# Kernel optimization log

Measured on AMD Instinct MI355X. Metric: run time of the kernel, lower is better.

The kernel has to match this reference:

```python
import jax, jax.numpy as jnp
import numpy as np

WS = 8        # window_size
NH = 8        # num_heads
LN_EPS = 1e-5

# static relative-position index table [WS*WS, WS*WS], values in [0, (2*WS-1)**2)
def _rel_index(ws):
    coords = np.arange(ws)
    grid = np.stack(np.meshgrid(coords, coords, indexing='ij')).reshape(2, -1)  # [2, W2]
    rel = grid[:, :, None] - grid[:, None, :]            # [2, W2, W2]
    rel = rel.transpose(1, 2, 0).copy()                   # [W2, W2, 2]
    rel[..., 0] += ws - 1
    rel[..., 1] += ws - 1
    rel[..., 0] *= 2 * ws - 1
    return rel.sum(-1)                                    # [W2, W2]

REL_IDX = jnp.asarray(_rel_index(WS))


def _ln(x):
    # LayerNorm without affine params (elementwise_affine=False)
    mu = jnp.mean(x, axis=-1, keepdims=True)
    var = jnp.var(x, axis=-1, keepdims=True)
    return (x - mu) * jax.lax.rsqrt(var + LN_EPS)


def setup_inputs() -> dict:
    key = jax.random.key(0)
    ks = jax.random.split(key, 16)
    B, Hg, Wg, C = 8, 64, 64, 256
    L = Hg * Wg
    s = 0.02
    inp = {
        'x': jax.random.normal(ks[0], (B, L, C), jnp.float32),
        't_embed': jax.random.normal(ks[1], (B, C), jnp.float32),
        'H': Hg,
        'W': Wg,
        'adaln1_w': s * jax.random.normal(ks[2], (C, 2 * C), jnp.float32),
        'adaln1_b': jnp.zeros((2 * C,), jnp.float32),
        'adaln2_w': s * jax.random.normal(ks[3], (C, 2 * C), jnp.float32),
        'adaln2_b': jnp.zeros((2 * C,), jnp.float32),
        'bias_table': s * jax.random.normal(ks[4], ((2 * WS - 1) ** 2, NH), jnp.float32),
        'q_w': s * jax.random.normal(ks[5], (C, C), jnp.float32),
        'q_b': jnp.zeros((C,), jnp.float32),
        'k_w': s * jax.random.normal(ks[6], (C, C), jnp.float32),
        'k_b': jnp.zeros((C,), jnp.float32),
        'v_w': s * jax.random.normal(ks[7], (C, C), jnp.float32),
        'v_b': jnp.zeros((C,), jnp.float32),
        'o_w': s * jax.random.normal(ks[8], (C, C), jnp.float32),
        'o_b': jnp.zeros((C,), jnp.float32),
        'ffn1_w': s * jax.random.normal(ks[9], (C, 4 * C), jnp.float32),
        'ffn1_b': jnp.zeros((4 * C,), jnp.float32),
        'ffn2_w': s * jax.random.normal(ks[10], (4 * C, C), jnp.float32),
        'ffn2_b': jnp.zeros((C,), jnp.float32),
    }
    return inp


def reference(x, t_embed, H, W, adaln1_w, adaln1_b, adaln2_w, adaln2_b,
              bias_table, q_w, q_b, k_w, k_b, v_w, v_b, o_w, o_b,
              ffn1_w, ffn1_b, ffn2_w, ffn2_b):
    B, L, C = x.shape
    d = C // NH
    W2 = WS * WS
    sh = WS // 2  # cyclic shift (shifted=True)

    # --- AdaLN1 ---
    ss = t_embed @ adaln1_w + adaln1_b              # [B, 2C]
    scale, shift = jnp.split(ss, 2, axis=-1)
    xn = _ln(x) * (1.0 + scale[:, None, :]) + shift[:, None, :]

    # --- shifted window partition ---
    xg = xn.reshape(B, H, W, C)
    xg = jnp.roll(xg, (-sh, -sh), axis=(1, 2))
    xw = xg.reshape(B, H // WS, WS, W // WS, WS, C).transpose(0, 1, 3, 2, 4, 5)
    xw = xw.reshape(-1, W2, C)                       # [nwB, W2, C]
    nwB = xw.shape[0]

    # --- window attention with relative position bias ---
    q = (xw @ q_w + q_b).reshape(nwB, W2, NH, d).transpose(0, 2, 1, 3)
    k = (xw @ k_w + k_b).reshape(nwB, W2, NH, d).transpose(0, 2, 1, 3)
    v = (xw @ v_w + v_b).reshape(nwB, W2, NH, d).transpose(0, 2, 1, 3)
    logits = jnp.einsum('whqd,whkd->whqk', q, k) * (d ** -0.5)
    bias = bias_table[REL_IDX.reshape(-1)].reshape(W2, W2, NH).transpose(2, 0, 1)
    logits = logits + bias[None].astype(logits.dtype)
    attn = jax.nn.softmax(logits, axis=-1)
    out = jnp.einsum('whqk,whkd->whqd', attn, v).transpose(0, 2, 1, 3).reshape(nwB, W2, C)
    out = out @ o_w + o_b

    # --- window reverse + unshift ---
    xm = out.reshape(B, H // WS, W // WS, WS, WS, C).transpose(0, 1, 3, 2, 4, 5)
    xm = xm.reshape(B, H, W, C)
    xm = jnp.roll(xm, (sh, sh), axis=(1, 2))
    x = x + xm.reshape(B, L, C)

    # --- AdaLN2 + FFN (GELU exact, matching torch nn.GELU) ---
    ss2 = t_embed @ adaln2_w + adaln2_b
    sc2, sh2 = jnp.split(ss2, 2, axis=-1)
    xn2 = _ln(x) * (1.0 + sc2[:, None, :]) + sh2[:, None, :]
    h = jax.nn.gelu(xn2 @ ffn1_w + ffn1_b, approximate=False)
    x = x + (h @ ffn2_w + ffn2_b)
    return x
```

## Files before the change

### kernel.cpp

```cpp
#include <hip/hip_runtime.h>
#include <math.h>

#define WS_ 8
#define NH_ 8
#define C_ 256
#define B_ 8
#define M_ 32768
#define SH_ 4
#define LN_EPS 1e-5f
#define SL_ 8388608

typedef __attribute__((ext_vector_type(8))) short bf16x8;
typedef __attribute__((ext_vector_type(4))) float f32x4;

__device__ inline float b2f(unsigned short u) {
    union { unsigned int i; float f; } c; c.i = ((unsigned int)u) << 16; return c.f;
}
__device__ inline unsigned short f2b(float f) {
    union { unsigned int i; float f; } c; c.f = f;
    unsigned int u = c.i;
    return (unsigned short)((u + 0x7FFFu + ((u >> 16) & 1u)) >> 16);
}
__device__ inline float gelu_f(float x) {
    float t = 1.59576912160573f * (x + 0.044715f * x * x * x);
    return x / (1.f + __expf(-t));
}

__global__ void prep_k(const float* __restrict__ qw, const float* __restrict__ kw,
                       const float* __restrict__ vw, const float* __restrict__ ow,
                       const float* __restrict__ f1w, const float* __restrict__ f2w,
                       const float* __restrict__ qb, const float* __restrict__ kb,
                       const float* __restrict__ vb, const float* __restrict__ bt,
                       const float* __restrict__ te,
                       const float* __restrict__ a1w, const float* __restrict__ a1b,
                       const float* __restrict__ a2w, const float* __restrict__ a2b,
                       unsigned short* __restrict__ qkvT, unsigned short* __restrict__ oT,
                       unsigned short* __restrict__ f1T, unsigned short* __restrict__ f2T,
                       float* __restrict__ qkvB, float* __restrict__ bias_full,
                       float* __restrict__ ss1, float* __restrict__ ss2) {
    int t = blockIdx.x * 256 + threadIdx.x;
    if (t < 196608) {
        int n = t >> 8, k = t & 255;
        const float* w = n < 256 ? qw : (n < 512 ? kw : vw);
        qkvT[t] = f2b(w[k * 256 + (n & 255)]);
    } else if (t < 262144) {
        int i = t - 196608; int n = i >> 8, k = i & 255;
        oT[i] = f2b(ow[k * 256 + n]);
    } else if (t < 524288) {
        int i = t - 262144; int n = i >> 8, k = i & 255;
        f1T[i] = f2b(f1w[k * 1024 + n]);
    } else if (t < 786432) {
        int i = t - 524288; int n = i >> 10, k = i & 1023;
        f2T[i] = f2b(f2w[k * 256 + n]);
    } else if (t < 787200) {
        int i = t - 786432;
        qkvB[i] = i < 256 ? qb[i] : (i < 512 ? kb[i - 256] : vb[i - 512]);
    } else if (t < 819968) {
        int i = t - 787200;
        int head = i >> 12, qk = i & 4095;
        int q = qk >> 6, k = qk & 63;
        int qh = q >> 3, qw2 = q & 7, kh = k >> 3, kw2 = k & 7;
        bias_full[i] = bt[((qh - kh + 7) * 15 + (qw2 - kw2 + 7)) * 8 + head];
    } else if (t < 828160) {
        int i = t - 819968;
        int which = i >> 12;
        int rem = i & 4095;
        int b = rem >> 9, col = rem & 511;
        const float* w = which ? a2w : a1w;
        const float* bb = which ? a2b : a1b;
        const float* tr = te + b * C_;
        float acc = bb[col];
        for (int k = 0; k < C_; ++k) acc += tr[k] * w[k * 512 + col];
        (which ? ss2 : ss1)[b * 512 + col] = acc;
    }
}

__global__ __launch_bounds__(256) void ln_win_k(const float* __restrict__ x,
                                                const float* __restrict__ ss,
                                                unsigned short* __restrict__ xw) {
    int t = blockIdx.x * 4 + (threadIdx.x >> 6);
    int lane = threadIdx.x & 63;
    int b = t >> 12, rem = t & 4095;
    int hg = rem >> 6, wg = rem & 63;
    int hs = (hg + SH_) & 63, wsrc = (wg + SH_) & 63;
    size_t src = ((size_t)b << 12) + (hs << 6) + wsrc;
    float4 v = *(const float4*)&x[src * C_ + lane * 4];
    float s = v.x + v.y + v.z + v.w;
    float s2 = v.x * v.x + v.y * v.y + v.z * v.z + v.w * v.w;
#pragma unroll
    for (int m = 1; m < 64; m <<= 1) { s += __shfl_xor(s, m); s2 += __shfl_xor(s2, m); }
    float mu = s * (1.f / 256.f);
    float rstd = rsqrtf(s2 * (1.f / 256.f) - mu * mu + LN_EPS);
    float4 sc = *(const float4*)&ss[b * 512 + lane * 4];
    float4 sh = *(const float4*)&ss[b * 512 + 256 + lane * 4];
    int win = (b << 6) + ((hg >> 3) << 3) + (wg >> 3);
    int pos = ((hg & 7) << 3) + (wg & 7);
    ushort4 pk;
    pk.x = f2b((v.x - mu) * rstd * (1.f + sc.x) + sh.x);
    pk.y = f2b((v.y - mu) * rstd * (1.f + sc.y) + sh.y);
    pk.z = f2b((v.z - mu) * rstd * (1.f + sc.z) + sh.z);
    pk.w = f2b((v.w - mu) * rstd * (1.f + sc.w) + sh.w);
    *(ushort4*)(xw + (size_t)(win * 64 + pos) * C_ + lane * 4) = pk;
}

__global__ __launch_bounds__(256) void ln_k(const float* __restrict__ x,
                                            const float* __restrict__ ss,
                                            unsigned short* __restrict__ y_out) {
    int t = blockIdx.x * 4 + (threadIdx.x >> 6);
    int lane = threadIdx.x & 63;
    int b = t >> 12;
    float4 v = *(const float4*)&x[(size_t)t * C_ + lane * 4];
    float s = v.x + v.y + v.z + v.w;
    float s2 = v.x * v.x + v.y * v.y + v.z * v.z + v.w * v.w;
#pragma unroll
    for (int m = 1; m < 64; m <<= 1) { s += __shfl_xor(s, m); s2 += __shfl_xor(s2, m); }
    float mu = s * (1.f / 256.f);
    float rstd = rsqrtf(s2 * (1.f / 256.f) - mu * mu + LN_EPS);
    float4 sc = *(const float4*)&ss[b * 512 + lane * 4];
    float4 sh = *(const float4*)&ss[b * 512 + 256 + lane * 4];
    ushort4 pk;
    pk.x = f2b((v.x - mu) * rstd * (1.f + sc.x) + sh.x);
    pk.y = f2b((v.y - mu) * rstd * (1.f + sc.y) + sh.y);
    pk.z = f2b((v.z - mu) * rstd * (1.f + sc.z) + sh.z);
    pk.w = f2b((v.w - mu) * rstd * (1.f + sc.w) + sh.w);
    *(ushort4*)(y_out + (size_t)t * C_ + lane * 4) = pk;
}

template <int KDIM, int MODE, int NT, int MINW>
__global__ __launch_bounds__(256, MINW) void gemm_bf16_k(
    const unsigned short* __restrict__ A, const unsigned short* __restrict__ Bt,
    const float* __restrict__ bias, const float* __restrict__ res,
    void* __restrict__ Cout, int Nout) {
    __shared__ __align__(16) unsigned short As[2][2][4096];
    __shared__ __align__(16) unsigned short Bs[2][2][4096];
    const int blk = blockIdx.x;
    const int xcd = blk & 7;
    const int idx = blk >> 3;
    const int mt = xcd + ((idx / NT) << 3);
    const int nt = idx % NT;
    const int bm = mt * 128, bn = nt * 128;
    const int tid = threadIdx.x;
    const int w = tid >> 6, lane = tid & 63;
    const int quad = lane >> 4, l16 = lane & 15;
    const int wm = (w >> 1) * 64, wn = (w & 1) * 64;
    const int srow = lane >> 2;
    const int qlog = ((lane & 3) ^ ((lane >> 3) & 3)) << 3;
    const int rsw = ((l16 >> 1) & 3) << 3;

    f32x4 acc[4][4] = {};

    auto stage = [&](int buf, int k0) {
#pragma unroll
        for (int h = 0; h < 2; ++h) {
#pragma unroll
            for (int j = 0; j < 2; ++j) {
                int r = j * 64 + w * 16 + srow;
                const unsigned short* ga = A + (size_t)(bm + r) * KDIM + k0 + h * 32 + qlog;
                unsigned short* la = &As[buf][h][j * 2048 + w * 512 + lane * 8];
                __builtin_amdgcn_global_load_lds(
                    (const __attribute__((address_space(1))) void*)ga,
                    (__attribute__((address_space(3))) void*)la, 16, 0, 0);
                const unsigned short* gb = Bt + (size_t)(bn + r) * KDIM + k0 + h * 32 + qlog;
                unsigned short* lb = &Bs[buf][h][j * 2048 + w * 512 + lane * 8];
                __builtin_amdgcn_global_load_lds(
                    (const __attribute__((address_space(1))) void*)gb,
                    (__attribute__((address_space(3))) void*)lb, 16, 0, 0);
            }
        }
    };

    constexpr int NK = KDIM / 64;
    stage(0, 0);
    asm volatile("s_waitcnt vmcnt(0)" ::: "memory");
    __builtin_amdgcn_s_barrier();

#pragma unroll
    for (int ks = 0; ks < NK; ++ks) {
        const int cur = ks & 1;
        if (ks + 1 < NK) stage(cur ^ 1, (ks + 1) * 64);
#pragma unroll
        for (int h = 0; h < 2; ++h) {
            bf16x8 af[4], bfr[4];
#pragma unroll
            for (int i = 0; i < 4; ++i)
                af[i] = *(const bf16x8*)&As[cur][h][(wm + i * 16 + l16) * 32 + ((quad << 3) ^ rsw)];
#pragma unroll
            for (int j = 0; j < 4; ++j)
                bfr[j] = *(const bf16x8*)&Bs[cur][h][(wn + j * 16 + l16) * 32 + ((quad << 3) ^ rsw)];
#pragma unroll
            for (int i = 0; i < 4; ++i)
#pragma unroll
                for (int j = 0; j < 4; ++j)
                    acc[i][j] = __builtin_amdgcn_mfma_f32_16x16x32_bf16(
                        bfr[j], af[i], acc[i][j], 0, 0, 0);
        }
        if (ks + 1 < NK) {
            asm volatile("s_waitcnt vmcnt(0)" ::: "memory");
            __builtin_amdgcn_s_barrier();
        }
    }

#pragma unroll
    for (int i = 0; i < 4; ++i) {
        const int row = bm + wm + i * 16 + l16;
        size_t rowbase = 0;
        if (MODE == 0) {
            int win = row >> 6, pos = row & 63;
            rowbase = (size_t)win * 16384 + pos * 32;
        } else if (MODE == 1) {
            int win = row >> 6, pos = row & 63;
            int b = win >> 6, wh = (win >> 3) & 7, ww = win & 7;
            int hg = (wh << 3) + (pos >> 3), wg = (ww << 3) + (pos & 7);
            int hd = (hg + SH_) & 63, wd = (wg + SH_) & 63;
            rowbase = (((size_t)b << 12) + (hd << 6) + wd) * C_;
        } else {
            rowbase = (size_t)row * Nout;
        }
#pragma unroll
        for (int j = 0; j < 4; ++j) {
            const int col = bn + wn + j * 16 + quad * 4;
            float4 bv = *(const float4*)&bias[col];
            float v0 = acc[i][j][0] + bv.x, v1 = acc[i][j][1] + bv.y;
            float v2 = acc[i][j][2] + bv.z, v3 = acc[i][j][3] + bv.w;
            if (MODE == 0) {
                int which = col >> 8, head = (col >> 5) & 7, dc = col & 31;
                ushort4 pk = {f2b(v0), f2b(v1), f2b(v2), f2b(v3)};
                *(ushort4*)((unsigned short*)Cout + (size_t)which * SL_ + rowbase +
                            head * 2048 + dc) = pk;
            } else if (MODE == 1) {
                float4 rv = *(const float4*)&res[rowbase + col];
                float4 ov = {v0 + rv.x, v1 + rv.y, v2 + rv.z, v3 + rv.w};
                *(float4*)&((float*)Cout)[rowbase + col] = ov;
            } else if (MODE == 2) {
                ushort4 pk = {f2b(gelu_f(v0)), f2b(gelu_f(v1)),
                              f2b(gelu_f(v2)), f2b(gelu_f(v3))};
                *(ushort4*)((unsigned short*)Cout + rowbase + col) = pk;
            } else {
                float4 rv = *(const float4*)&res[rowbase + col];
                float4 ov = {v0 + rv.x, v1 + rv.y, v2 + rv.z, v3 + rv.w};
                *(float4*)&((float*)Cout)[rowbase + col] = ov;
            }
        }
    }
}

__global__ __launch_bounds__(256) void attn_mfma_k(
    const unsigned short* __restrict__ qkv, const float* __restrict__ bias_full,
    unsigned short* __restrict__ attn_out) {
    __shared__ __align__(16) unsigned short Pb[4][64 * 66];
    __shared__ __align__(16) unsigned short Vt[4][32 * 66];
    const int w = threadIdx.x >> 6, lane = threadIdx.x & 63;
    const int wh = blockIdx.x * 4 + w;
    const int win = wh >> 3, head = wh & 7;
    const int quad = lane >> 4, l16 = lane & 15;

    const unsigned short* qp = qkv + (size_t)win * 16384 + head * 2048;
    const unsigned short* kp = qp + SL_;
    const unsigned short* vp = qp + 2 * (size_t)SL_;

    {
        const uint4* v4 = (const uint4*)(vp + lane * 32);
        unsigned short* dst = &Vt[w][0];
#pragma unroll
        for (int c = 0; c < 4; ++c) {
            uint4 u = v4[c];
            unsigned int uu[4] = {u.x, u.y, u.z, u.w};
#pragma unroll
            for (int p = 0; p < 4; ++p) {
                int d0 = c * 8 + p * 2;
                dst[d0 * 66 + lane] = (unsigned short)(uu[p] & 0xffff);
                dst[(d0 + 1) * 66 + lane] = (unsigned short)(uu[p] >> 16);
            }
        }
    }

    bf16x8 qf[4], kf[4];
#pragma unroll
    for (int i = 0; i < 4; ++i) {
        qf[i] = *(const bf16x8*)(qp + (i * 16 + l16) * 32 + quad * 8);
        kf[i] = *(const bf16x8*)(kp + (i * 16 + l16) * 32 + quad * 8);
    }

    f32x4 s[4][4] = {};
#pragma unroll
    for (int i = 0; i < 4; ++i)
#pragma unroll
        for (int j = 0; j < 4; ++j)
            s[i][j] = __builtin_amdgcn_mfma_f32_16x16x32_bf16(qf[i], kf[j], s[i][j], 0, 0, 0);

    const float scale = 0.17677669529663687f;
    const float* bf = bias_full + head * 4096;
    float rs[4][4];
#pragma unroll
    for (int i = 0; i < 4; ++i) {
#pragma unroll
        for (int r = 0; r < 4; ++r) {
            int row = i * 16 + quad * 4 + r;
            float acc = 0.f;
#pragma unroll
            for (int j = 0; j < 4; ++j) {
                float e = __expf(s[i][j][r] * scale + bf[row * 64 + j * 16 + l16]);
                s[i][j][r] = e;
                acc += e;
            }
#pragma unroll
            for (int msk = 1; msk < 16; msk <<= 1) acc += __shfl_xor(acc, msk);
            rs[i][r] = 1.f / acc;
        }
    }

#pragma unroll
    for (int i = 0; i < 4; ++i)
#pragma unroll
        for (int j = 0; j < 4; ++j)
#pragma unroll
            for (int r = 0; r < 4; ++r)
                Pb[w][(i * 16 + quad * 4 + r) * 66 + j * 16 + l16] = f2b(s[i][j][r]);

    __syncthreads();

    f32x4 o[4][2] = {};
#pragma unroll
    for (int st = 0; st < 2; ++st) {
        bf16x8 bv[2];
#pragma unroll
        for (int jo = 0; jo < 2; ++jo)
            bv[jo] = *(const bf16x8*)&Vt[w][(jo * 16 + l16) * 66 + st * 32 + quad * 8];
#pragma unroll
        for (int i = 0; i < 4; ++i) {
            bf16x8 af = *(const bf16x8*)&Pb[w][(i * 16 + l16) * 66 + st * 32 + quad * 8];
#pragma unroll
            for (int jo = 0; jo < 2; ++jo)
                o[i][jo] = __builtin_amdgcn_mfma_f32_16x16x32_bf16(af, bv[jo], o[i][jo], 0, 0, 0);
        }
    }

#pragma unroll
    for (int i = 0; i < 4; ++i)
#pragma unroll
        for (int jo = 0; jo < 2; ++jo)
#pragma unroll
            for (int r = 0; r < 4; ++r) {
                int row = i * 16 + quad * 4 + r;
                int d = jo * 16 + l16;
                attn_out[((size_t)(win * 64 + row)) * C_ + head * 32 + d] =
                    f2b(o[i][jo][r] * rs[i][r]);
            }
}

extern "C" void kernel_launch(void* const* d_in, const int* in_sizes, int n_in,
                              void* d_out, int out_size, void* d_ws, size_t ws_size,
                              hipStream_t stream) {
    const float* x        = (const float*)d_in[0];
    const float* t_embed  = (const float*)d_in[1];
    const float* adaln1_w = (const float*)d_in[4];
    const float* adaln1_b = (const float*)d_in[5];
    const float* adaln2_w = (const float*)d_in[6];
    const float* adaln2_b = (const float*)d_in[7];
    const float* bt       = (const float*)d_in[8];
    const float* q_w = (const float*)d_in[9],  *q_b = (const float*)d_in[10];
    const float* k_w = (const float*)d_in[11], *k_b = (const float*)d_in[12];
    const float* v_w = (const float*)d_in[13], *v_b = (const float*)d_in[14];
    const float* o_w = (const float*)d_in[15], *o_b = (const float*)d_in[16];
    const float* f1_w = (const float*)d_in[17], *f1_b = (const float*)d_in[18];
    const float* f2_w = (const float*)d_in[19], *f2_b = (const float*)d_in[20];
    float* out = (float*)d_out;

    char* wsb = (char*)d_ws;
    float* ss1            = (float*)(wsb + 0);
    float* ss2            = (float*)(wsb + 16384);
    float* qkvB           = (float*)(wsb + 32768);
    unsigned short* qkvT  = (unsigned short*)(wsb + 36864);
    unsigned short* oT    = (unsigned short*)(wsb + 430080);
    unsigned short* f1T   = (unsigned short*)(wsb + 561152);
    unsigned short* f2T   = (unsigned short*)(wsb + 1085440);
    float* bias_full      = (float*)(wsb + 1609728);
    unsigned short* xw    = (unsigned short*)(wsb + 2097152);
    unsigned short* qkv   = (unsigned short*)(wsb + 18874368);
    unsigned short* attn  = (unsigned short*)(wsb + 69206016);
    unsigned short* xn2   = xw;
    unsigned short* hbuf  = qkv;
    float* x1             = (float*)(wsb + 85983232);

    prep_k<<<3235, 256, 0, stream>>>(q_w, k_w, v_w, o_w, f1_w, f2_w, q_b, k_b, v_b, bt,
                                     t_embed, adaln1_w, adaln1_b, adaln2_w, adaln2_b,
                                     qkvT, oT, f1T, f2T, qkvB, bias_full, ss1, ss2);
    ln_win_k<<<8192, 256, 0, stream>>>(x, ss1, xw);

    gemm_bf16_k<256, 0, 6, 2><<<1536, 256, 0, stream>>>(xw, qkvT, qkvB, nullptr, qkv, 768);

    attn_mfma_k<<<1024, 256, 0, stream>>>(qkv, bias_full, attn);

    gemm_bf16_k<256, 1, 2, 2><<<512, 256, 0, stream>>>(attn, oT, o_b, x, x1, 256);
    ln_k<<<8192, 256, 0, stream>>>(x1, ss2, xn2);
    gemm_bf16_k<256, 2, 8, 2><<<2048, 256, 0, stream>>>(xn2, f1T, f1_b, nullptr, hbuf, 1024);
    gemm_bf16_k<1024, 3, 2, 2><<<512, 256, 0, stream>>>(hbuf, f2T, f2_b, x1, out, 256);
}
```

Measured before the change: 276.5 us.

## Restructure GEMMs with full-K A tiles in LDS, direct B loads, and fused LN2

Replaces the 128x128 double-buffered GEMM with a 512-thread kernel that computes 128x256 output tiles. Each block stages a full 256-wide K chunk of A into swizzled LDS and reads B fragments straight from global memory. The O-projection GEMM now covers a full row of 256 columns, so it also computes LayerNorm plus AdaLN2 in its epilogue through an LDS reduction, and the separate ln_k kernel is removed. This saves one launch and one full read of x1. The cost is a 64KB+ LDS footprint that limits occupancy, and uncached B reads from global memory may add latency.

Result: slower. 317.4 us (+14.8%).

```diff
diff --git a/kernel.cpp b/kernel.cpp
--- a/kernel.cpp
+++ b/kernel.cpp
@@ -103,122 +103,176 @@
     *(ushort4*)(xw + (size_t)(win * 64 + pos) * C_ + lane * 4) = pk;
 }
 
-__global__ __launch_bounds__(256) void ln_k(const float* __restrict__ x,
-                                            const float* __restrict__ ss,
-                                            unsigned short* __restrict__ y_out) {
-    int t = blockIdx.x * 4 + (threadIdx.x >> 6);
-    int lane = threadIdx.x & 63;
-    int b = t >> 12;
-    float4 v = *(const float4*)&x[(size_t)t * C_ + lane * 4];
-    float s = v.x + v.y + v.z + v.w;
-    float s2 = v.x * v.x + v.y * v.y + v.z * v.z + v.w * v.w;
-#pragma unroll
-    for (int m = 1; m < 64; m <<= 1) { s += __shfl_xor(s, m); s2 += __shfl_xor(s2, m); }
-    float mu = s * (1.f / 256.f);
-    float rstd = rsqrtf(s2 * (1.f / 256.f) - mu * mu + LN_EPS);
-    float4 sc = *(const float4*)&ss[b * 512 + lane * 4];
-    float4 sh = *(const float4*)&ss[b * 512 + 256 + lane * 4];
-    ushort4 pk;
-    pk.x = f2b((v.x - mu) * rstd * (1.f + sc.x) + sh.x);
-    pk.y = f2b((v.y - mu) * rstd * (1.f + sc.y) + sh.y);
-    pk.z = f2b((v.z - mu) * rstd * (1.f + sc.z) + sh.z);
-    pk.w = f2b((v.w - mu) * rstd * (1.f + sc.w) + sh.w);
-    *(ushort4*)(y_out + (size_t)t * C_ + lane * 4) = pk;
-}
-
-template <int KDIM, int MODE, int NT, int MINW>
-__global__ __launch_bounds__(256, MINW) void gemm_bf16_k(
+template <int KDIM, int MODE, int NT>
+__global__ __launch_bounds__(512, 2) void gemmv_k(
     const unsigned short* __restrict__ A, const unsigned short* __restrict__ Bt,
     const float* __restrict__ bias, const float* __restrict__ res,
-    void* __restrict__ Cout, int Nout) {
-    __shared__ __align__(16) unsigned short As[2][2][4096];
-    __shared__ __align__(16) unsigned short Bs[2][2][4096];
+    void* __restrict__ Cout, const float* __restrict__ ss2,
+    unsigned short* __restrict__ xn2out, int Nout) {
+    constexpr int NCH = KDIM / 256;
+    constexpr int NBUF = (NCH > 1) ? 2 : 1;
+    __shared__ __align__(16) unsigned short As[NBUF][128 * 256];
+
     const int blk = blockIdx.x;
     const int xcd = blk & 7;
     const int idx = blk >> 3;
     const int mt = xcd + ((idx / NT) << 3);
     const int nt = idx % NT;
-    const int bm = mt * 128, bn = nt * 128;
+    const int bm = mt * 128, bn = nt * 256;
     const int tid = threadIdx.x;
     const int w = tid >> 6, lane = tid & 63;
     const int quad = lane >> 4, l16 = lane & 15;
-    const int wm = (w >> 1) * 64, wn = (w & 1) * 64;
-    const int srow = lane >> 2;
-    const int qlog = ((lane & 3) ^ ((lane >> 3) & 3)) << 3;
-    const int rsw = ((l16 >> 1) & 3) << 3;
+    const int wrow = (w >> 2) * 64;
+    const int wcol = (w & 3) * 64;
+    const int srow16 = tid >> 5;
+    const int sc = tid & 31;
 
     f32x4 acc[4][4] = {};
 
-    auto stage = [&](int buf, int k0) {
-#pragma unroll
-        for (int h = 0; h < 2; ++h) {
-#pragma unroll
-            for (int j = 0; j < 2; ++j) {
-                int r = j * 64 + w * 16 + srow;
-                const unsigned short* ga = A + (size_t)(bm + r) * KDIM + k0 + h * 32 + qlog;
-                unsigned short* la = &As[buf][h][j * 2048 + w * 512 + lane * 8];
-                __builtin_amdgcn_global_load_lds(
-                    (const __attribute__((address_space(1))) void*)ga,
-                    (__attribute__((address_space(3))) void*)la, 16, 0, 0);
-                const unsigned short* gb = Bt + (size_t)(bn + r) * KDIM + k0 + h * 32 + qlog;
-                unsigned short* lb = &Bs[buf][h][j * 2048 + w * 512 + lane * 8];
-                __builtin_amdgcn_global_load_lds(
-                    (const __attribute__((address_space(1))) void*)gb,
-                    (__attribute__((address_space(3))) void*)lb, 16, 0, 0);
-            }
+    auto stageA = [&](int buf, int kc) {
+#pragma unroll
+        for (int p = 0; p < 8; ++p) {
+            int row = p * 16 + srow16;
+            int g = sc ^ (row & 7);
+            const unsigned short* ga = A + (size_t)(bm + row) * KDIM + kc * 256 + g * 8;
+            unsigned short* la = &As[buf][row * 256 + sc * 8];
+            __builtin_amdgcn_global_load_lds(
+                (const __attribute__((address_space(1))) void*)ga,
+                (__attribute__((address_space(3))) void*)la, 16, 0, 0);
         }
     };
 
-    constexpr int NK = KDIM / 64;
-    stage(0, 0);
-    asm volatile("s_waitcnt vmcnt(0)" ::: "memory");
-    __builtin_amdgcn_s_barrier();
-
-#pragma unroll
-    for (int ks = 0; ks < NK; ++ks) {
-        const int cur = ks & 1;
-        if (ks + 1 < NK) stage(cur ^ 1, (ks + 1) * 64);
-#pragma unroll
-        for (int h = 0; h < 2; ++h) {
-            bf16x8 af[4], bfr[4];
-#pragma unroll
-            for (int i = 0; i < 4; ++i)
-                af[i] = *(const bf16x8*)&As[cur][h][(wm + i * 16 + l16) * 32 + ((quad << 3) ^ rsw)];
+    auto computeC = [&](int buf, int kc) {
+        const unsigned short* bp = Bt + (size_t)(bn + wcol + l16) * KDIM + kc * 256 + quad * 8;
+#pragma unroll
+        for (int k8 = 0; k8 < 8; ++k8) {
+            bf16x8 bfr[4], af[4];
 #pragma unroll
             for (int j = 0; j < 4; ++j)
-                bfr[j] = *(const bf16x8*)&Bs[cur][h][(wn + j * 16 + l16) * 32 + ((quad << 3) ^ rsw)];
+                bfr[j] = *(const bf16x8*)(bp + (size_t)j * 16 * KDIM + k8 * 32);
+#pragma unroll
+            for (int i = 0; i < 4; ++i) {
+                int row = wrow + i * 16 + l16;
+                int cidx = (k8 * 4 + quad) ^ (row & 7);
+                af[i] = *(const bf16x8*)&As[buf][row * 256 + cidx * 8];
+            }
+            __builtin_amdgcn_s_setprio(1);
 #pragma unroll
             for (int i = 0; i < 4; ++i)
 #pragma unroll
                 for (int j = 0; j < 4; ++j)
                     acc[i][j] = __builtin_amdgcn_mfma_f32_16x16x32_bf16(
                         bfr[j], af[i], acc[i][j], 0, 0, 0);
-        }
-        if (ks + 1 < NK) {
-            asm volatile("s_waitcnt vmcnt(0)" ::: "memory");
-            __builtin_amdgcn_s_barrier();
-        }
+            __builtin_amdgcn_s_setprio(0);
+        }
+    };
+
+    stageA(0, 0);
+    asm volatile("s_waitcnt vmcnt(0)" ::: "memory");
+    __builtin_amdgcn_s_barrier();
+    if constexpr (NCH == 1) {
+        computeC(0, 0);
+    } else {
+#pragma unroll
+        for (int c = 0; c < NCH; ++c) {
+            if (c + 1 < NCH) stageA((c + 1) & 1, c + 1);
+            computeC(c & 1, c);
+            if (c + 1 < NCH) {
+                asm volatile("s_waitcnt vmcnt(0)" ::: "memory");
+                __builtin_amdgcn_s_barrier();
+            }
+        }
+    }
+
+    if (MODE == 1) {
+        float ps[4], ps2[4];
+#pragma unroll
+        for (int i = 0; i < 4; ++i) {
+            const int row = bm + wrow + i * 16 + l16;
+            int win = row >> 6, pos = row & 63;
+            int b = win >> 6, wh = (win >> 3) & 7, ww = win & 7;
+            int hg = (wh << 3) + (pos >> 3), wg = (ww << 3) + (pos & 7);
+            int hd = (hg + SH_) & 63, wd = (wg + SH_) & 63;
+            size_t rowbase = (((size_t)b << 12) + (hd << 6) + wd) * C_;
+            float s = 0.f, s2 = 0.f;
+#pragma unroll
+            for (int j = 0; j < 4; ++j) {
+                const int col = bn + wcol + j * 16 + quad * 4;
+                float4 bv = *(const float4*)&bias[col];
+                float4 rv = *(const float4*)&res[rowbase + col];
+                float4 ov = {acc[i][j][0] + bv.x + rv.x, acc[i][j][1] + bv.y + rv.y,
+                             acc[i][j][2] + bv.z + rv.z, acc[i][j][3] + bv.w + rv.w};
+                *(float4*)&((float*)Cout)[rowbase + col] = ov;
+                acc[i][j][0] = ov.x; acc[i][j][1] = ov.y;
+                acc[i][j][2] = ov.z; acc[i][j][3] = ov.w;
+                s += ov.x + ov.y + ov.z + ov.w;
+                s2 += ov.x * ov.x + ov.y * ov.y + ov.z * ov.z + ov.w * ov.w;
+            }
+            ps[i] = s; ps2[i] = s2;
+        }
+#pragma unroll
+        for (int i = 0; i < 4; ++i) {
+            ps[i] += __shfl_xor(ps[i], 16);  ps[i] += __shfl_xor(ps[i], 32);
+            ps2[i] += __shfl_xor(ps2[i], 16); ps2[i] += __shfl_xor(ps2[i], 32);
+        }
+        float* sred = (float*)&As[0][0];
+        asm volatile("s_waitcnt lgkmcnt(0)" ::: "memory");
+        __builtin_amdgcn_s_barrier();
+        if (quad == 0) {
+#pragma unroll
+            for (int i = 0; i < 4; ++i) {
+                int r = i * 16 + l16;
+                sred[(w * 64 + r) * 2 + 0] = ps[i];
+                sred[(w * 64 + r) * 2 + 1] = ps2[i];
+            }
+        }
+        __builtin_amdgcn_s_barrier();
+#pragma unroll
+        for (int i = 0; i < 4; ++i) {
+            int r = i * 16 + l16;
+            float s = 0.f, s2 = 0.f;
+#pragma unroll
+            for (int cw = 0; cw < 4; ++cw) {
+                s  += sred[(((w >> 2) * 4 + cw) * 64 + r) * 2 + 0];
+                s2 += sred[(((w >> 2) * 4 + cw) * 64 + r) * 2 + 1];
+            }
+            float mu = s * (1.f / 256.f);
+            float rstd = rsqrtf(s2 * (1.f / 256.f) - mu * mu + LN_EPS);
+            const int row = bm + wrow + i * 16 + l16;
+            int win = row >> 6, pos = row & 63;
+            int b = win >> 6, wh = (win >> 3) & 7, ww = win & 7;
+            int hg = (wh << 3) + (pos >> 3), wg = (ww << 3) + (pos & 7);
+            int hd = (hg + SH_) & 63, wd = (wg + SH_) & 63;
+            size_t rowbase = (((size_t)b << 12) + (hd << 6) + wd) * C_;
+#pragma unroll
+            for (int j = 0; j < 4; ++j) {
+                const int col = bn + wcol + j * 16 + quad * 4;
+                float4 scv = *(const float4*)&ss2[b * 512 + col];
+                float4 shv = *(const float4*)&ss2[b * 512 + 256 + col];
+                ushort4 pk;
+                pk.x = f2b((acc[i][j][0] - mu) * rstd * (1.f + scv.x) + shv.x);
+                pk.y = f2b((acc[i][j][1] - mu) * rstd * (1.f + scv.y) + shv.y);
+                pk.z = f2b((acc[i][j][2] - mu) * rstd * (1.f + scv.z) + shv.z);
+                pk.w = f2b((acc[i][j][3] - mu) * rstd * (1.f + scv.w) + shv.w);
+                *(ushort4*)(xn2out + rowbase + col) = pk;
+            }
+        }
+        return;
     }
 
 #pragma unroll
     for (int i = 0; i < 4; ++i) {
-        const int row = bm + wm + i * 16 + l16;
+        const int row = bm + wrow + i * 16 + l16;
         size_t rowbase = 0;
         if (MODE == 0) {
             int win = row >> 6, pos = row & 63;
             rowbase = (size_t)win * 16384 + pos * 32;
-        } else if (MODE == 1) {
-            int win = row >> 6, pos = row & 63;
-            int b = win >> 6, wh = (win >> 3) & 7, ww = win & 7;
-            int hg = (wh << 3) + (pos >> 3), wg = (ww << 3) + (pos & 7);
-            int hd = (hg + SH_) & 63, wd = (wg + SH_) & 63;
-            rowbase = (((size_t)b << 12) + (hd << 6) + wd) * C_;
         } else {
             rowbase = (size_t)row * Nout;
         }
 #pragma unroll
         for (int j = 0; j < 4; ++j) {
-            const int col = bn + wn + j * 16 + quad * 4;
+            const int col = bn + wcol + j * 16 + quad * 4;
             float4 bv = *(const float4*)&bias[col];
             float v0 = acc[i][j][0] + bv.x, v1 = acc[i][j][1] + bv.y;
             float v2 = acc[i][j][2] + bv.z, v3 = acc[i][j][3] + bv.w;
@@ -227,10 +281,6 @@
                 ushort4 pk = {f2b(v0), f2b(v1), f2b(v2), f2b(v3)};
                 *(ushort4*)((unsigned short*)Cout + (size_t)which * SL_ + rowbase +
                             head * 2048 + dc) = pk;
-            } else if (MODE == 1) {
-                float4 rv = *(const float4*)&res[rowbase + col];
-                float4 ov = {v0 + rv.x, v1 + rv.y, v2 + rv.z, v3 + rv.w};
-                *(float4*)&((float*)Cout)[rowbase + col] = ov;
             } else if (MODE == 2) {
                 ushort4 pk = {f2b(gelu_f(v0)), f2b(gelu_f(v1)),
                               f2b(gelu_f(v2)), f2b(gelu_f(v3))};
@@ -387,12 +437,15 @@
                                      qkvT, oT, f1T, f2T, qkvB, bias_full, ss1, ss2);
     ln_win_k<<<8192, 256, 0, stream>>>(x, ss1, xw);
 
-    gemm_bf16_k<256, 0, 6, 2><<<1536, 256, 0, stream>>>(xw, qkvT, qkvB, nullptr, qkv, 768);
+    gemmv_k<256, 0, 3><<<768, 512, 0, stream>>>(xw, qkvT, qkvB, nullptr, qkv,
+                                                nullptr, nullptr, 768);
 
     attn_mfma_k<<<1024, 256, 0, stream>>>(qkv, bias_full, attn);
 
-    gemm_bf16_k<256, 1, 2, 2><<<512, 256, 0, stream>>>(attn, oT, o_b, x, x1, 256);
-    ln_k<<<8192, 256, 0, stream>>>(x1, ss2, xn2);
-    gemm_bf16_k<256, 2, 8, 2><<<2048, 256, 0, stream>>>(xn2, f1T, f1_b, nullptr, hbuf, 1024);
-    gemm_bf16_k<1024, 3, 2, 2><<<512, 256, 0, stream>>>(hbuf, f2T, f2_b, x1, out, 256);
-}
+    gemmv_k<256, 1, 1><<<256, 512, 0, stream>>>(attn, oT, o_b, x, x1,
+                                                ss2, xn2, 256);
+    gemmv_k<256, 2, 4><<<1024, 512, 0, stream>>>(xn2, f1T, f1_b, nullptr, hbuf,
+                                                 nullptr, nullptr, 1024);
+    gemmv_k<1024, 3, 1><<<256, 512, 0, stream>>>(hbuf, f2T, f2_b, x1, out,
+                                                 nullptr, nullptr, 256);
+}
```
